# Kernel tuning notes

Hardware: AMD Instinct MI355X
Metric: run time of the kernel (lower is better)

Reference implementation:

```python
import jax, jax.numpy as jnp
import numpy as np

G = 512      # graphs per batch
PER = 800    # nodes per graph
N = G * PER  # total nodes
X = 256      # x_size (= h_size so layers compose)
H = 256      # h_size
VOCAB = 32000
NCLS = 104


def setup_inputs() -> dict:
    rng = np.random.default_rng(0)
    # Random tree per graph: node 0 is root, parent(i) uniform in [0, i)
    i_idx = np.arange(1, PER)
    parents = np.floor(rng.random((G, PER - 1)) * i_idx).astype(np.int64)
    base = (np.arange(G) * PER)[:, None]
    edge_dst = (parents + base).reshape(-1)                     # parent (message receiver)
    edge_src = (np.tile(np.arange(1, PER), (G, 1)) + base).reshape(-1)  # child
    E = edge_src.size
    child_count = np.bincount(edge_dst, minlength=N)
    # sort edges by (dst, src) so child position = rank among siblings
    order = np.lexsort((edge_src, edge_dst))
    edge_src = edge_src[order]
    edge_dst = edge_dst[order]
    starts = np.cumsum(child_count) - child_count
    pos = np.arange(E) - starts[edge_dst]
    n = child_count[edge_dst]
    # position-dependent interpolation coefficient: n==1 -> (W_l+W_r)/2 i.e. alpha=0.5
    alpha = np.where(n == 1, 0.5, pos / np.maximum(n - 1, 1)).astype(np.float32)

    node_type = rng.integers(0, VOCAB, N).astype(np.int32)
    graph_ids = np.repeat(np.arange(G), PER).astype(np.int32)

    key = jax.random.key(0)
    ks = jax.random.split(key, 6)
    s = 0.05
    emb = jax.random.normal(ks[0], (VOCAB, X), jnp.float32) * s
    W_left = jax.random.normal(ks[1], (X, H), jnp.float32) * s
    W_right = jax.random.normal(ks[2], (X, H), jnp.float32) * s
    W_top = jax.random.normal(ks[3], (X, H), jnp.float32) * s
    b_conv = jnp.zeros((H,), jnp.float32)
    gate_w = jax.random.normal(ks[4], (H, 1), jnp.float32) * s
    gate_b = jnp.zeros((1,), jnp.float32)
    cls_w = jax.random.normal(ks[5], (H, NCLS), jnp.float32) * s
    cls_b = jnp.zeros((NCLS,), jnp.float32)

    return dict(
        node_type=jnp.asarray(node_type), edge_src=jnp.asarray(edge_src.astype(np.int32)),
        edge_dst=jnp.asarray(edge_dst.astype(np.int32)), alpha=jnp.asarray(alpha),
        child_count=jnp.asarray(child_count.astype(np.int32)), graph_ids=jnp.asarray(graph_ids),
        emb=emb, W_left=W_left, W_right=W_right, W_top=W_top, b_conv=b_conv,
        gate_w=gate_w, gate_b=gate_b, cls_w=cls_w, cls_b=cls_b,
    )


def reference(node_type, edge_src, edge_dst, alpha, child_count, graph_ids,
              emb, W_left, W_right, W_top, b_conv,
              gate_w, gate_b, cls_w, cls_b):
    h = emb[node_type]                                  # [N, X]
    # TBCNN conv layer: sum_i ((1-a_i) W_left + a_i W_right) h_child_i
    #                 = (sum (1-a_i) h_i) W_left + (sum a_i h_i) W_right
    h_src = h[edge_src]                                 # [E, X]
    left = jax.ops.segment_sum(h_src * (1.0 - alpha)[:, None], edge_dst, num_segments=N)
    right = jax.ops.segment_sum(h_src * alpha[:, None], edge_dst, num_segments=N)
    conv = jax.nn.relu(left @ W_left + right @ W_right + h @ W_top + b_conv)
    # nodes without children receive no message -> keep embedding (DGL semantics)
    h = jnp.where((child_count > 0)[:, None], conv, h)  # [N, H]

    # GlobalAttentionPooling: per-graph softmax over gate scores
    gate = h @ gate_w + gate_b                          # [N, 1]
    gmax = jax.ops.segment_max(gate, graph_ids, num_segments=G)
    e = jnp.exp(gate - gmax[graph_ids])
    denom = jax.ops.segment_sum(e, graph_ids, num_segments=G)
    attn = e / denom[graph_ids]                         # [N, 1]
    pooled = jax.ops.segment_sum(h * attn, graph_ids, num_segments=G)  # [G, H]

    return pooled @ cls_w + cls_b                       # [G, NCLS]
```

## Files before the change

kernel.cpp:

```cpp
#include <hip/hip_runtime.h>
#include <stdint.h>

#define XH   256
#define NCLS 104

typedef __attribute__((ext_vector_type(8))) short          short8;
typedef __attribute__((ext_vector_type(4))) float          floatx4;
typedef __attribute__((ext_vector_type(4))) unsigned short ushort4b;
typedef __attribute__((ext_vector_type(8))) unsigned short ushort8b;

__device__ __forceinline__ float bf2f(unsigned short u) {
    unsigned v = ((unsigned)u) << 16;
    return __builtin_bit_cast(float, v);
}
__device__ __forceinline__ unsigned short f2bf(float f) {
    unsigned v = __builtin_bit_cast(unsigned, f);
    unsigned r = (v + 0x7fffu + ((v >> 16) & 1u)) >> 16;
    return (unsigned short)r;
}
__device__ __forceinline__ void gll16(const void* g, void* l) {
    __builtin_amdgcn_global_load_lds(
        (const __attribute__((address_space(1))) unsigned*)g,
        (__attribute__((address_space(3))) unsigned*)l, 16, 0, 0);
}

__global__ __launch_bounds__(256)
void k_prep(const float* __restrict__ emb, const float* __restrict__ Wl,
            const float* __restrict__ Wr, const float* __restrict__ Wt,
            const int* __restrict__ edge_src, const int* __restrict__ edge_dst,
            const float* __restrict__ alpha, const int* __restrict__ node_type,
            unsigned short* __restrict__ embh, unsigned short* __restrict__ Btw,
            int2* __restrict__ epk, int* __restrict__ row_start,
            int vocab, int E) {
    int idx = blockIdx.x * 256 + threadIdx.x;
    int nA = vocab * (XH / 4);
    if (idx < nA) {
        floatx4 f = *(const floatx4*)&emb[(size_t)idx * 4];
        ushort4b u;
        #pragma unroll
        for (int i = 0; i < 4; i++) u[i] = f2bf(f[i]);
        *(ushort4b*)&embh[(size_t)idx * 4] = u;
        return;
    }
    idx -= nA;
    int nB = 3 * XH * XH;
    if (idx < nB) {
        int n = idx >> 8, k = idx & 255;
        int m, c;
        if (n < 512) { m = n & 1; c = n >> 1; }
        else         { m = 2;     c = n - 512; }
        const float* W = (m == 0) ? Wl : (m == 1) ? Wr : Wt;
        Btw[idx] = f2bf(W[k * XH + c]);
        return;
    }
    idx -= nB;
    if (idx < E) {
        int s = edge_src[idx];
        int2 p;
        p.x = node_type[s] * 512;
        p.y = __float_as_int(alpha[idx]);
        epk[idx] = p;
        int d = edge_dst[idx];
        if (idx == 0 || edge_dst[idx - 1] != d) row_start[d] = idx;
    }
}

__global__ __launch_bounds__(256)
void k_gemm(const unsigned short* __restrict__ embh,
            const unsigned short* __restrict__ Btw,
            const float* __restrict__ b_conv,
            unsigned short* __restrict__ Ylr, unsigned short* __restrict__ Yt) {
    const int m0 = blockIdx.x * 128;
    const int n0 = blockIdx.y * 128;
    const int tid  = threadIdx.x;
    const int lane = tid & 63;
    const int wv   = tid >> 6;
    const int mw   = wv >> 1;
    const int nw   = wv & 1;
    const int quad = lane >> 4;
    const int l15  = lane & 15;

    __shared__ __align__(16) unsigned short Ab[128 * 32];
    __shared__ __align__(16) unsigned short Bb[128 * 32];

    floatx4 acc[4][4];
    #pragma unroll
    for (int i = 0; i < 4; i++)
        #pragma unroll
        for (int j = 0; j < 4; j++) acc[i][j] = floatx4{0.f, 0.f, 0.f, 0.f};

    const int lq = lane >> 2;
    const int lb = (lane & 3) * 16;

    for (int kc = 0; kc < 8; kc++) {
        #pragma unroll
        for (int i = 0; i < 2; i++) {
            int issue = wv * 2 + i;
            int row   = issue * 16 + lq;
            gll16((const char*)embh + (size_t)(m0 + row) * 512 + kc * 64 + lb,
                  (char*)Ab + issue * 1024);
            gll16((const char*)Btw + (size_t)(n0 + row) * 512 + kc * 64 + lb,
                  (char*)Bb + issue * 1024);
        }
        __syncthreads();
        short8 a[4];
        #pragma unroll
        for (int mt = 0; mt < 4; mt++)
            a[mt] = *(const short8*)((const char*)Ab + (mw * 64 + mt * 16 + l15) * 64 + quad * 16);
        #pragma unroll
        for (int nt = 0; nt < 4; nt++) {
            short8 b = *(const short8*)((const char*)Bb + (nw * 64 + nt * 16 + l15) * 64 + quad * 16);
            #pragma unroll
            for (int mt = 0; mt < 4; mt++)
                acc[mt][nt] = __builtin_amdgcn_mfma_f32_16x16x32_bf16(a[mt], b, acc[mt][nt], 0, 0, 0);
        }
        __syncthreads();
    }

    const bool isT = (n0 >= 512);
    #pragma unroll
    for (int nt = 0; nt < 4; nt++) {
        int col = n0 + nw * 64 + nt * 16 + l15;
        float bias = isT ? b_conv[col - 512] : 0.f;
        #pragma unroll
        for (int mt = 0; mt < 4; mt++) {
            #pragma unroll
            for (int r = 0; r < 4; r++) {
                int row = m0 + mw * 64 + mt * 16 + quad * 4 + r;
                unsigned short val = f2bf(acc[mt][nt][r] + bias);
                if (isT) Yt[(size_t)row * XH + (col - 512)] = val;
                else     Ylr[(size_t)row * 512 + col] = val;
            }
        }
    }
}

__global__ __launch_bounds__(1024, 8)
void k_graph(const int* __restrict__ node_type, const int* __restrict__ child_count,
             const unsigned short* __restrict__ embh,
             const unsigned short* __restrict__ Ylr, const unsigned short* __restrict__ Yt,
             const int2* __restrict__ epk, const int* __restrict__ row_start,
             const float* __restrict__ gate_w, const float* __restrict__ gate_b,
             const float* __restrict__ cls_w, const float* __restrict__ cls_b,
             float* __restrict__ out, int PER) {
    const int g    = blockIdx.x;
    const int tid  = threadIdx.x;
    const int lane = tid & 63;
    const int wv   = tid >> 6;
    const int base = g * PER;

    __shared__ float pw[16 * XH];
    __shared__ float ds[16];
    __shared__ float pooled[XH];

    float gw4[4];
    #pragma unroll
    for (int i = 0; i < 4; i++) gw4[i] = gate_w[4 * lane + i];
    const float gb = gate_b[0];

    float acc4[4] = {0.f, 0.f, 0.f, 0.f};
    float dsum = 0.f;

    int vg = base + wv;
    int c  = child_count[vg];
    int tv = node_type[vg];
    int rs = row_start[vg];

    for (int v = wv; v < PER; v += 16) {
        int cn = 0, tvn = 0, rsn = 0;
        if (v + 16 < PER) {
            cn  = child_count[vg + 16];
            tvn = node_type[vg + 16];
            rsn = row_start[vg + 16];
        }

        float h4[4];
        if (c == 0) {
            ushort4b hv = *(const ushort4b*)&embh[(size_t)tv * XH + 4 * lane];
            #pragma unroll
            for (int i = 0; i < 4; i++) h4[i] = bf2f(hv[i]);
        } else {
            ushort4b yt = *(const ushort4b*)&Yt[(size_t)tv * XH + 4 * lane];
            float s4[4] = {0.f, 0.f, 0.f, 0.f};
            int e = rs, e1 = rs + c;
            for (; e + 2 <= e1; e += 2) {
                int2 p0 = epk[e], p1 = epk[e + 1];
                ushort8b w0 = *(const ushort8b*)&Ylr[(size_t)p0.x + 8 * lane];
                ushort8b w1 = *(const ushort8b*)&Ylr[(size_t)p1.x + 8 * lane];
                float a0 = __int_as_float(p0.y), a1 = __int_as_float(p1.y);
                #pragma unroll
                for (int i = 0; i < 4; i++) {
                    float l0 = bf2f(w0[2 * i]), r0 = bf2f(w0[2 * i + 1]);
                    s4[i] += l0 + a0 * (r0 - l0);
                }
                #pragma unroll
                for (int i = 0; i < 4; i++) {
                    float l1 = bf2f(w1[2 * i]), r1 = bf2f(w1[2 * i + 1]);
                    s4[i] += l1 + a1 * (r1 - l1);
                }
            }
            if (e < e1) {
                int2 p0 = epk[e];
                ushort8b w0 = *(const ushort8b*)&Ylr[(size_t)p0.x + 8 * lane];
                float a0 = __int_as_float(p0.y);
                #pragma unroll
                for (int i = 0; i < 4; i++) {
                    float l0 = bf2f(w0[2 * i]), r0 = bf2f(w0[2 * i + 1]);
                    s4[i] += l0 + a0 * (r0 - l0);
                }
            }
            #pragma unroll
            for (int i = 0; i < 4; i++)
                h4[i] = fmaxf(s4[i] + bf2f(yt[i]), 0.f);
        }

        float sg = h4[0] * gw4[0] + h4[1] * gw4[1] + h4[2] * gw4[2] + h4[3] * gw4[3];
        #pragma unroll
        for (int o = 1; o < 64; o <<= 1) sg += __shfl_xor(sg, o);
        float ew = __expf(sg + gb);
        dsum += ew;
        #pragma unroll
        for (int i = 0; i < 4; i++) acc4[i] += ew * h4[i];

        c = cn; tv = tvn; rs = rsn; vg += 16;
    }

    #pragma unroll
    for (int i = 0; i < 4; i++) pw[wv * XH + 4 * lane + i] = acc4[i];
    if (lane == 0) ds[wv] = dsum;
    __syncthreads();

    if (tid < XH) {
        float p = 0.f, d = 0.f;
        #pragma unroll
        for (int w = 0; w < 16; w++) p += pw[w * XH + tid];
        #pragma unroll
        for (int w = 0; w < 16; w++) d += ds[w];
        pooled[tid] = p / d;
    }
    __syncthreads();

    if (tid < NCLS) {
        float o = cls_b[tid];
        #pragma unroll 8
        for (int k = 0; k < XH; k++) o += pooled[k] * cls_w[k * NCLS + tid];
        out[g * NCLS + tid] = o;
    }
}

extern "C" void kernel_launch(void* const* d_in, const int* in_sizes, int n_in,
                              void* d_out, int out_size, void* d_ws, size_t ws_size,
                              hipStream_t stream) {
    const int*   node_type   = (const int*)d_in[0];
    const int*   edge_src    = (const int*)d_in[1];
    const int*   edge_dst    = (const int*)d_in[2];
    const float* alpha       = (const float*)d_in[3];
    const int*   child_count = (const int*)d_in[4];
    const float* emb         = (const float*)d_in[6];
    const float* Wl          = (const float*)d_in[7];
    const float* Wr          = (const float*)d_in[8];
    const float* Wt          = (const float*)d_in[9];
    const float* b_conv      = (const float*)d_in[10];
    const float* gate_w      = (const float*)d_in[11];
    const float* gate_b      = (const float*)d_in[12];
    const float* cls_w       = (const float*)d_in[13];
    const float* cls_b       = (const float*)d_in[14];

    const int N     = in_sizes[0];
    const int E     = in_sizes[1];
    const int vocab = in_sizes[6] / XH;
    const int G     = out_size / NCLS;
    const int PER   = N / G;

    unsigned short* Ylr  = (unsigned short*)d_ws;
    unsigned short* Yt   = Ylr + (size_t)vocab * 512;
    unsigned short* embh = Yt + (size_t)vocab * XH;
    unsigned short* Btw  = embh + (size_t)vocab * XH;
    int2*           epk  = (int2*)(Btw + 3 * XH * XH);
    int*            row_start = (int*)(epk + E);

    const int nprep = vocab * (XH / 4) + 3 * XH * XH + E;
    hipLaunchKernelGGL(k_prep, dim3((nprep + 255) / 256), dim3(256), 0, stream,
                       emb, Wl, Wr, Wt, edge_src, edge_dst, alpha, node_type,
                       embh, Btw, epk, row_start, vocab, E);

    hipLaunchKernelGGL(k_gemm, dim3(vocab / 128, 6), dim3(256), 0, stream,
                       embh, Btw, b_conv, Ylr, Yt);

    hipLaunchKernelGGL(k_graph, dim3(G), dim3(1024), 0, stream,
                       node_type, child_count, embh, Ylr, Yt, epk, row_start,
                       gate_w, gate_b, cls_w, cls_b, (float*)d_out, PER);
}
```

Baseline: 243.5 us.

## Fuse embedding conversion and edge packing into GEMM, switch to fp16 with fdot2

Moves the fp32-to-half conversion of the embedding table out of a separate prep pass and into the GEMM's A-tile load, with the ng==0 column blocks also writing the fp16 embedding copy. Edge packing now runs as extra blocks of the GEMM launch. The prep kernel shrinks to weight transposition only. Storage and MFMA switch from bf16 to fp16, and edge alphas are pre-packed as half2 (1-a, a) so the graph kernel interpolates with one fdot2 per pair. The aims are to avoid a full extra pass over the embedding table and to cut ALU work in the gather loop, at the cost of fp16 range limits and a small precision change.

```diff
diff --git a/kernel.cpp b/kernel.cpp
--- a/kernel.cpp
+++ b/kernel.cpp
@@ -4,75 +4,71 @@
 #define XH   256
 #define NCLS 104
 
-typedef __attribute__((ext_vector_type(8))) short          short8;
-typedef __attribute__((ext_vector_type(4))) float          floatx4;
-typedef __attribute__((ext_vector_type(4))) unsigned short ushort4b;
-typedef __attribute__((ext_vector_type(8))) unsigned short ushort8b;
-
-__device__ __forceinline__ float bf2f(unsigned short u) {
-    unsigned v = ((unsigned)u) << 16;
-    return __builtin_bit_cast(float, v);
-}
-__device__ __forceinline__ unsigned short f2bf(float f) {
-    unsigned v = __builtin_bit_cast(unsigned, f);
-    unsigned r = (v + 0x7fffu + ((v >> 16) & 1u)) >> 16;
-    return (unsigned short)r;
-}
+typedef _Float16 half2v __attribute__((ext_vector_type(2)));
+typedef _Float16 half4v __attribute__((ext_vector_type(4)));
+typedef _Float16 half8v __attribute__((ext_vector_type(8)));
+typedef __attribute__((ext_vector_type(4))) float floatx4;
+
 __device__ __forceinline__ void gll16(const void* g, void* l) {
     __builtin_amdgcn_global_load_lds(
         (const __attribute__((address_space(1))) unsigned*)g,
         (__attribute__((address_space(3))) unsigned*)l, 16, 0, 0);
 }
 
+__device__ __forceinline__ float fdot2f(half2v a, half2v b, float c) {
+#if __has_builtin(__builtin_amdgcn_fdot2)
+    return __builtin_amdgcn_fdot2(a, b, c, false);
+#else
+    return c + (float)a[0] * (float)b[0] + (float)a[1] * (float)b[1];
+#endif
+}
+
 __global__ __launch_bounds__(256)
-void k_prep(const float* __restrict__ emb, const float* __restrict__ Wl,
-            const float* __restrict__ Wr, const float* __restrict__ Wt,
+void k_prep(const float* __restrict__ Wl, const float* __restrict__ Wr,
+            const float* __restrict__ Wt, _Float16* __restrict__ Btw) {
+    int idx = blockIdx.x * 256 + threadIdx.x;
+    if (idx >= 3 * XH * XH) return;
+    int n = idx >> 8, k = idx & 255;
+    int m, c;
+    if (n < 512) { m = n & 1; c = n >> 1; }
+    else         { m = 2;     c = n - 512; }
+    const float* W = (m == 0) ? Wl : (m == 1) ? Wr : Wt;
+    Btw[idx] = (_Float16)W[k * XH + c];
+}
+
+__global__ __launch_bounds__(256)
+void k_gemm(const float* __restrict__ emb, const _Float16* __restrict__ Btw,
+            const float* __restrict__ b_conv,
             const int* __restrict__ edge_src, const int* __restrict__ edge_dst,
             const float* __restrict__ alpha, const int* __restrict__ node_type,
-            unsigned short* __restrict__ embh, unsigned short* __restrict__ Btw,
-            int2* __restrict__ epk, int* __restrict__ row_start,
-            int vocab, int E) {
-    int idx = blockIdx.x * 256 + threadIdx.x;
-    int nA = vocab * (XH / 4);
-    if (idx < nA) {
-        floatx4 f = *(const floatx4*)&emb[(size_t)idx * 4];
-        ushort4b u;
-        #pragma unroll
-        for (int i = 0; i < 4; i++) u[i] = f2bf(f[i]);
-        *(ushort4b*)&embh[(size_t)idx * 4] = u;
+            _Float16* __restrict__ Ylr, _Float16* __restrict__ Yt,
+            _Float16* __restrict__ embf, int2* __restrict__ epk,
+            int* __restrict__ row_start, int Mb, int E) {
+    __shared__ __align__(16) _Float16 Ab[128 * 32];
+    __shared__ __align__(16) _Float16 Bb[128 * 32];
+
+    const int bx  = blockIdx.x;
+    const int tid = threadIdx.x;
+
+    if (bx >= Mb * 6) {
+        int e = (bx - Mb * 6) * 256 + tid;
+        if (e < E) {
+            int s = edge_src[e];
+            float a = alpha[e];
+            half2v w = { (_Float16)(1.f - a), (_Float16)a };
+            int2 p;
+            p.x = node_type[s] * 512;
+            p.y = __builtin_bit_cast(int, w);
+            epk[e] = p;
+            int d = edge_dst[e];
+            if (e == 0 || edge_dst[e - 1] != d) row_start[d] = e;
+        }
         return;
     }
-    idx -= nA;
-    int nB = 3 * XH * XH;
-    if (idx < nB) {
-        int n = idx >> 8, k = idx & 255;
-        int m, c;
-        if (n < 512) { m = n & 1; c = n >> 1; }
-        else         { m = 2;     c = n - 512; }
-        const float* W = (m == 0) ? Wl : (m == 1) ? Wr : Wt;
-        Btw[idx] = f2bf(W[k * XH + c]);
-        return;
-    }
-    idx -= nB;
-    if (idx < E) {
-        int s = edge_src[idx];
-        int2 p;
-        p.x = node_type[s] * 512;
-        p.y = __float_as_int(alpha[idx]);
-        epk[idx] = p;
-        int d = edge_dst[idx];
-        if (idx == 0 || edge_dst[idx - 1] != d) row_start[d] = idx;
-    }
-}
-
-__global__ __launch_bounds__(256)
-void k_gemm(const unsigned short* __restrict__ embh,
-            const unsigned short* __restrict__ Btw,
-            const float* __restrict__ b_conv,
-            unsigned short* __restrict__ Ylr, unsigned short* __restrict__ Yt) {
-    const int m0 = blockIdx.x * 128;
-    const int n0 = blockIdx.y * 128;
-    const int tid  = threadIdx.x;
+
+    const int m0   = (bx / 6) * 128;
+    const int ng   = bx % 6;
+    const int n0   = ng * 128;
     const int lane = tid & 63;
     const int wv   = tid >> 6;
     const int mw   = wv >> 1;
@@ -80,15 +76,14 @@
     const int quad = lane >> 4;
     const int l15  = lane & 15;
 
-    __shared__ __align__(16) unsigned short Ab[128 * 32];
-    __shared__ __align__(16) unsigned short Bb[128 * 32];
-
     floatx4 acc[4][4];
     #pragma unroll
     for (int i = 0; i < 4; i++)
         #pragma unroll
         for (int j = 0; j < 4; j++) acc[i][j] = floatx4{0.f, 0.f, 0.f, 0.f};
 
+    const int ar = tid >> 1;
+    const int ah = (tid & 1) * 16;
     const int lq = lane >> 2;
     const int lb = (lane & 3) * 16;
 
@@ -97,22 +92,42 @@
         for (int i = 0; i < 2; i++) {
             int issue = wv * 2 + i;
             int row   = issue * 16 + lq;
-            gll16((const char*)embh + (size_t)(m0 + row) * 512 + kc * 64 + lb,
-                  (char*)Ab + issue * 1024);
             gll16((const char*)Btw + (size_t)(n0 + row) * 512 + kc * 64 + lb,
                   (char*)Bb + issue * 1024);
         }
+        {
+            const float* ga = &emb[(size_t)(m0 + ar) * XH + kc * 32 + ah];
+            floatx4 f0 = *(const floatx4*)ga;
+            floatx4 f1 = *(const floatx4*)(ga + 4);
+            floatx4 f2 = *(const floatx4*)(ga + 8);
+            floatx4 f3 = *(const floatx4*)(ga + 12);
+            half8v h0, h1;
+            #pragma unroll
+            for (int i = 0; i < 4; i++) {
+                h0[i]     = (_Float16)f0[i];
+                h0[4 + i] = (_Float16)f1[i];
+                h1[i]     = (_Float16)f2[i];
+                h1[4 + i] = (_Float16)f3[i];
+            }
+            *(half8v*)&Ab[ar * 32 + ah]     = h0;
+            *(half8v*)&Ab[ar * 32 + ah + 8] = h1;
+            if (ng == 0) {
+                _Float16* ep = &embf[(size_t)(m0 + ar) * XH + kc * 32 + ah];
+                *(half8v*)ep       = h0;
+                *(half8v*)(ep + 8) = h1;
+            }
+        }
         __syncthreads();
-        short8 a[4];
+        half8v a[4];
         #pragma unroll
         for (int mt = 0; mt < 4; mt++)
-            a[mt] = *(const short8*)((const char*)Ab + (mw * 64 + mt * 16 + l15) * 64 + quad * 16);
+            a[mt] = *(const half8v*)&Ab[(mw * 64 + mt * 16 + l15) * 32 + quad * 8];
         #pragma unroll
         for (int nt = 0; nt < 4; nt++) {
-            short8 b = *(const short8*)((const char*)Bb + (nw * 64 + nt * 16 + l15) * 64 + quad * 16);
+            half8v b = *(const half8v*)&Bb[(nw * 64 + nt * 16 + l15) * 32 + quad * 8];
             #pragma unroll
             for (int mt = 0; mt < 4; mt++)
-                acc[mt][nt] = __builtin_amdgcn_mfma_f32_16x16x32_bf16(a[mt], b, acc[mt][nt], 0, 0, 0);
+                acc[mt][nt] = __builtin_amdgcn_mfma_f32_16x16x32_f16(a[mt], b, acc[mt][nt], 0, 0, 0);
         }
         __syncthreads();
     }
@@ -127,7 +142,7 @@
             #pragma unroll
             for (int r = 0; r < 4; r++) {
                 int row = m0 + mw * 64 + mt * 16 + quad * 4 + r;
-                unsigned short val = f2bf(acc[mt][nt][r] + bias);
+                _Float16 val = (_Float16)(acc[mt][nt][r] + bias);
                 if (isT) Yt[(size_t)row * XH + (col - 512)] = val;
                 else     Ylr[(size_t)row * 512 + col] = val;
             }
@@ -137,8 +152,8 @@
 
 __global__ __launch_bounds__(1024, 8)
 void k_graph(const int* __restrict__ node_type, const int* __restrict__ child_count,
-             const unsigned short* __restrict__ embh,
-             const unsigned short* __restrict__ Ylr, const unsigned short* __restrict__ Yt,
+             const _Float16* __restrict__ embf,
+             const _Float16* __restrict__ Ylr, const _Float16* __restrict__ Yt,
              const int2* __restrict__ epk, const int* __restrict__ row_start,
              const float* __restrict__ gate_w, const float* __restrict__ gate_b,
              const float* __restrict__ cls_w, const float* __restrict__ cls_b,
@@ -176,42 +191,37 @@
 
         float h4[4];
         if (c == 0) {
-            ushort4b hv = *(const ushort4b*)&embh[(size_t)tv * XH + 4 * lane];
-            #pragma unroll
-            for (int i = 0; i < 4; i++) h4[i] = bf2f(hv[i]);
+            half4v hv = *(const half4v*)&embf[(size_t)tv * XH + 4 * lane];
+            #pragma unroll
+            for (int i = 0; i < 4; i++) h4[i] = (float)hv[i];
         } else {
-            ushort4b yt = *(const ushort4b*)&Yt[(size_t)tv * XH + 4 * lane];
+            half4v yt = *(const half4v*)&Yt[(size_t)tv * XH + 4 * lane];
             float s4[4] = {0.f, 0.f, 0.f, 0.f};
             int e = rs, e1 = rs + c;
             for (; e + 2 <= e1; e += 2) {
                 int2 p0 = epk[e], p1 = epk[e + 1];
-                ushort8b w0 = *(const ushort8b*)&Ylr[(size_t)p0.x + 8 * lane];
-                ushort8b w1 = *(const ushort8b*)&Ylr[(size_t)p1.x + 8 * lane];
-                float a0 = __int_as_float(p0.y), a1 = __int_as_float(p1.y);
+                half8v y0 = *(const half8v*)&Ylr[(size_t)p0.x + 8 * lane];
+                half8v y1 = *(const half8v*)&Ylr[(size_t)p1.x + 8 * lane];
+                half2v w0 = __builtin_bit_cast(half2v, p0.y);
+                half2v w1 = __builtin_bit_cast(half2v, p1.y);
                 #pragma unroll
-                for (int i = 0; i < 4; i++) {
-                    float l0 = bf2f(w0[2 * i]), r0 = bf2f(w0[2 * i + 1]);
-                    s4[i] += l0 + a0 * (r0 - l0);
-                }
+                for (int i = 0; i < 4; i++)
+                    s4[i] = fdot2f(half2v{y0[2 * i], y0[2 * i + 1]}, w0, s4[i]);
                 #pragma unroll
-                for (int i = 0; i < 4; i++) {
-                    float l1 = bf2f(w1[2 * i]), r1 = bf2f(w1[2 * i + 1]);
-                    s4[i] += l1 + a1 * (r1 - l1);
-                }
+                for (int i = 0; i < 4; i++)
+                    s4[i] = fdot2f(half2v{y1[2 * i], y1[2 * i + 1]}, w1, s4[i]);
             }
             if (e < e1) {
                 int2 p0 = epk[e];
-                ushort8b w0 = *(const ushort8b*)&Ylr[(size_t)p0.x + 8 * lane];
-                float a0 = __int_as_float(p0.y);
+                half8v y0 = *(const half8v*)&Ylr[(size_t)p0.x + 8 * lane];
+                half2v w0 = __builtin_bit_cast(half2v, p0.y);
                 #pragma unroll
-                for (int i = 0; i < 4; i++) {
-                    float l0 = bf2f(w0[2 * i]), r0 = bf2f(w0[2 * i + 1]);
-                    s4[i] += l0 + a0 * (r0 - l0);
-                }
+                for (int i = 0; i < 4; i++)
+                    s4[i] = fdot2f(half2v{y0[2 * i], y0[2 * i + 1]}, w0, s4[i]);
             }
             #pragma unroll
             for (int i = 0; i < 4; i++)
-                h4[i] = fmaxf(s4[i] + bf2f(yt[i]), 0.f);
+                h4[i] = fmaxf(s4[i] + (float)yt[i], 0.f);
         }
 
         float sg = h4[0] * gw4[0] + h4[1] * gw4[1] + h4[2] * gw4[2] + h4[3] * gw4[3];
@@ -271,23 +281,24 @@
     const int vocab = in_sizes[6] / XH;
     const int G     = out_size / NCLS;
     const int PER   = N / G;
-
-    unsigned short* Ylr  = (unsigned short*)d_ws;
-    unsigned short* Yt   = Ylr + (size_t)vocab * 512;
-    unsigned short* embh = Yt + (size_t)vocab * XH;
-    unsigned short* Btw  = embh + (size_t)vocab * XH;
-    int2*           epk  = (int2*)(Btw + 3 * XH * XH);
-    int*            row_start = (int*)(epk + E);
-
-    const int nprep = vocab * (XH / 4) + 3 * XH * XH + E;
-    hipLaunchKernelGGL(k_prep, dim3((nprep + 255) / 256), dim3(256), 0, stream,
-                       emb, Wl, Wr, Wt, edge_src, edge_dst, alpha, node_type,
-                       embh, Btw, epk, row_start, vocab, E);
-
-    hipLaunchKernelGGL(k_gemm, dim3(vocab / 128, 6), dim3(256), 0, stream,
-                       embh, Btw, b_conv, Ylr, Yt);
+    const int Mb    = vocab / 128;
+    const int Eb    = (E + 255) / 256;
+
+    _Float16* Ylr  = (_Float16*)d_ws;
+    _Float16* Yt   = Ylr + (size_t)vocab * 512;
+    _Float16* embf = Yt + (size_t)vocab * XH;
+    _Float16* Btw  = embf + (size_t)vocab * XH;
+    int2*     epk  = (int2*)(Btw + 3 * XH * XH);
+    int*      row_start = (int*)(epk + E);
+
+    hipLaunchKernelGGL(k_prep, dim3((3 * XH * XH + 255) / 256), dim3(256), 0, stream,
+                       Wl, Wr, Wt, Btw);
+
+    hipLaunchKernelGGL(k_gemm, dim3(Mb * 6 + Eb), dim3(256), 0, stream,
+                       emb, Btw, b_conv, edge_src, edge_dst, alpha, node_type,
+                       Ylr, Yt, embf, epk, row_start, Mb, E);
 
     hipLaunchKernelGGL(k_graph, dim3(G), dim3(1024), 0, stream,
-                       node_type, child_count, embh, Ylr, Yt, epk, row_start,
+                       node_type, child_count, embf, Ylr, Yt, epk, row_start,
                        gate_w, gate_b, cls_w, cls_b, (float*)d_out, PER);
 }
```

After: 253.2 us. 1.04x slower.
